# Optimization experiments

Measured on AMD Instinct MI355X. Metric: run time of the kernel, lower is better.

Reference implementation:

```python
import jax, jax.numpy as jnp
import numpy as np

THRESHOLD = 0.5
NEG_POS_RATIO = 3
ALPHA = 1.0


def cxcy_to_xy(c):
    # (cx,cy,w,h) -> (xmin,ymin,xmax,ymax)
    return jnp.concatenate([c[..., :2] - c[..., 2:] / 2.0,
                            c[..., :2] + c[..., 2:] / 2.0], axis=-1)


def gcxgcy_to_cxcy(g, priors):
    # standard SSD decode with variances (10, 5)
    return jnp.concatenate([g[..., :2] * priors[..., 2:] / 10.0 + priors[..., :2],
                            jnp.exp(g[..., 2:] / 5.0) * priors[..., 2:]], axis=-1)


def jaccard(set1, set2):
    # set1: [n1,4], set2: [n2,4], xyxy -> IoU matrix [n1,n2]
    lo = jnp.maximum(set1[:, None, :2], set2[None, :, :2])
    hi = jnp.minimum(set1[:, None, 2:], set2[None, :, 2:])
    wh = jnp.clip(hi - lo, 0.0)
    inter = wh[..., 0] * wh[..., 1]
    a1 = (set1[:, 2] - set1[:, 0]) * (set1[:, 3] - set1[:, 1])
    a2 = (set2[:, 2] - set2[:, 0]) * (set2[:, 3] - set2[:, 1])
    return inter / (a1[:, None] + a2[None, :] - inter)


def match_one(b, l, priors_xy):
    # b: [n_obj,4] GT boxes, l: [n_obj] labels, priors_xy: [P,4]
    n_obj = b.shape[0]
    ov = jaccard(b, priors_xy)                      # [n_obj, P]
    obj_for_prior = jnp.argmax(ov, axis=0)          # [P]
    ov_for_prior = jnp.max(ov, axis=0)              # [P]
    prior_for_obj = jnp.argmax(ov, axis=1)          # [n_obj]
    # force each object to own its best prior
    obj_for_prior = obj_for_prior.at[prior_for_obj].set(jnp.arange(n_obj))
    ov_for_prior = ov_for_prior.at[prior_for_obj].set(1.0)
    lab = l[obj_for_prior]
    lab = jnp.where(ov_for_prior < THRESHOLD, 0, lab)
    return lab, b[obj_for_prior]


def ciou(b1, b2):
    # elementwise CIoU over [..., 4] xyxy boxes -> [...]
    w1 = b1[..., 2] - b1[..., 0]; h1 = b1[..., 3] - b1[..., 1]
    w2 = b2[..., 2] - b2[..., 0]; h2 = b2[..., 3] - b2[..., 1]
    area1 = w1 * h1; area2 = w2 * h2
    cx1 = (b1[..., 2] + b1[..., 0]) / 2; cy1 = (b1[..., 3] + b1[..., 1]) / 2
    cx2 = (b2[..., 2] + b2[..., 0]) / 2; cy2 = (b2[..., 3] + b2[..., 1]) / 2
    in_wh = jnp.clip(jnp.minimum(b1[..., 2:], b2[..., 2:]) - jnp.maximum(b1[..., :2], b2[..., :2]), 0.0)
    out_wh = jnp.clip(jnp.maximum(b1[..., 2:], b2[..., 2:]) - jnp.minimum(b1[..., :2], b2[..., :2]), 0.0)
    inner_diag = (cx2 - cx1) ** 2 + (cy2 - cy1) ** 2
    outer_diag = out_wh[..., 0] ** 2 + out_wh[..., 1] ** 2
    inner = in_wh[..., 0] * in_wh[..., 1]
    iou = inner / (area1 + area2 - inner)
    v = (4.0 / (np.pi ** 2)) * (jnp.arctan(w2 / h2) - jnp.arctan(w1 / h1)) ** 2
    alpha = jax.lax.stop_gradient(v / (1.0 - iou + v))  # torch.no_grad()
    return 1.0 - iou + inner_diag / outer_diag + alpha * v


def setup_inputs() -> dict:
    key = jax.random.key(0)
    ks = jax.random.split(key, 7)
    N, P, C, NOBJ = 32, 8732, 81, 24
    predicted_locs = jax.random.normal(ks[0], (N, P, 4), jnp.float32)
    predicted_scores = jax.random.normal(ks[1], (N, P, C), jnp.float32)
    mins = jax.random.uniform(ks[2], (N, NOBJ, 2), minval=0.0, maxval=0.7)
    sizes = jax.random.uniform(ks[3], (N, NOBJ, 2), minval=0.05, maxval=0.3)
    boxes = jnp.concatenate([mins, mins + sizes], axis=-1)  # well-formed xyxy
    labels = jax.random.randint(ks[4], (N, NOBJ), 1, C)      # 1..C-1 (0 = background)
    pc = jax.random.uniform(ks[5], (P, 2), minval=0.05, maxval=0.95)
    pwh = jax.random.uniform(ks[6], (P, 2), minval=0.05, maxval=0.5)
    priors_cxcy = jnp.concatenate([pc, pwh], axis=-1)
    return {"predicted_locs": predicted_locs, "predicted_scores": predicted_scores,
            "boxes": boxes, "labels": labels, "priors_cxcy": priors_cxcy}


def reference(predicted_locs, predicted_scores, boxes, labels, priors_cxcy):
    priors_xy = cxcy_to_xy(priors_cxcy)
    # per-image GT->prior matching (vectorized over batch)
    true_classes, decoded_true = jax.vmap(match_one, in_axes=(0, 0, None))(boxes, labels, priors_xy)
    decoded_pred = cxcy_to_xy(gcxgcy_to_cxcy(predicted_locs, priors_cxcy[None]))  # [N,P,4]
    pos = true_classes != 0                              # [N,P]
    posf = pos.astype(predicted_locs.dtype)
    n_pos_total = jnp.sum(posf)
    # localization: CIoU mean over positive priors
    loc_loss = jnp.sum(ciou(decoded_pred, decoded_true) * posf) / n_pos_total
    # confidence: CE per prior
    logp = jax.nn.log_softmax(predicted_scores, axis=-1)
    conf_all = -jnp.take_along_axis(logp, true_classes[..., None], axis=-1)[..., 0]  # [N,P]
    conf_pos_sum = jnp.sum(conf_all * posf)
    # hard negative mining: top (neg_pos_ratio * n_pos) negatives per image
    conf_neg = jnp.where(pos, 0.0, conf_all)
    conf_neg_sorted = -jnp.sort(-conf_neg, axis=1)       # descending
    n_hard = NEG_POS_RATIO * jnp.sum(pos, axis=1)        # [N]
    ranks = jnp.arange(conf_neg_sorted.shape[1])[None, :]
    hard_mask = (ranks < n_hard[:, None]).astype(conf_all.dtype)
    conf_hard_neg_sum = jnp.sum(conf_neg_sorted * hard_mask)
    conf_loss = (conf_hard_neg_sum + conf_pos_sum) / n_pos_total
    return conf_loss + ALPHA * loc_loss
```

## Files before the change

### kernel.cpp

```cpp
#include <hip/hip_runtime.h>
#include <math.h>

#define BLK  256
#define BLKM 1024

constexpr int N_IMG = 32;
constexpr int P_PRI = 8732;
constexpr int C_CLS = 81;
constexpr int N_OBJ = 24;
constexpr int RPB   = 64;
constexpr int PB2   = (P_PRI + RPB - 1) / RPB;
constexpr int NBLK2 = PB2 * N_IMG;

__global__ void k_obj_match(const float* __restrict__ boxes,
                            const float* __restrict__ priors,
                            int* __restrict__ prior_for_obj,
                            int* __restrict__ npos) {
    const int o = blockIdx.x;
    const int n = blockIdx.y;
    const int tid = threadIdx.x;

    if (o == 0 && tid == 0) npos[n] = 0;

    const float x1 = boxes[(n * N_OBJ + o) * 4 + 0];
    const float y1 = boxes[(n * N_OBJ + o) * 4 + 1];
    const float x2 = boxes[(n * N_OBJ + o) * 4 + 2];
    const float y2 = boxes[(n * N_OBJ + o) * 4 + 3];
    const float ab = (x2 - x1) * (y2 - y1);

    const float4* pr4 = (const float4*)priors;

    float bv = -1.0f;
    int   bi = P_PRI;
    for (int p = tid; p < P_PRI; p += BLK) {
        const float4 c = pr4[p];
        const float px1 = c.x - c.z / 2.0f, py1 = c.y - c.w / 2.0f;
        const float px2 = c.x + c.z / 2.0f, py2 = c.y + c.w / 2.0f;
        const float pa  = (px2 - px1) * (py2 - py1);
        const float lox = fmaxf(x1, px1), loy = fmaxf(y1, py1);
        const float hix = fminf(x2, px2), hiy = fminf(y2, py2);
        const float iw = fmaxf(hix - lox, 0.0f), ih = fmaxf(hiy - loy, 0.0f);
        const float inter = iw * ih;
        const float iou = inter / (ab + pa - inter);
        if (iou > bv) { bv = iou; bi = p; }
    }

    __shared__ float sv[BLK];
    __shared__ int   si[BLK];
    sv[tid] = bv; si[tid] = bi;
    __syncthreads();
    for (int s = BLK / 2; s > 0; s >>= 1) {
        if (tid < s) {
            const float v2 = sv[tid + s]; const int i2 = si[tid + s];
            if (v2 > sv[tid] || (v2 == sv[tid] && i2 < si[tid])) { sv[tid] = v2; si[tid] = i2; }
        }
        __syncthreads();
    }
    if (tid == 0) prior_for_obj[n * N_OBJ + o] = si[0];
}

__global__ void __launch_bounds__(BLK)
k_main(const float* __restrict__ locs,
       const float* __restrict__ scores,
       const float* __restrict__ boxes,
       const int*   __restrict__ labels,
       const float* __restrict__ priors,
       const int*   __restrict__ prior_for_obj,
       float* __restrict__ conf_neg,
       int*   __restrict__ npos,
       float* __restrict__ partial_conf,
       float* __restrict__ partial_loc) {
    __shared__ int   pfo[N_OBJ];
    __shared__ int   slab[N_OBJ];
    __shared__ float wred[4][4];

    const int n   = blockIdx.y;
    const int r0  = blockIdx.x * RPB;
    const int tid = threadIdx.x;
    const int rows = min(RPB, P_PRI - r0);

    if (tid < N_OBJ) pfo[tid] = prior_for_obj[n * N_OBJ + tid];
    if (tid >= 64 && tid < 64 + N_OBJ) slab[tid - 64] = labels[n * N_OBJ + (tid - 64)];

    const int row = tid >> 2;
    const int q   = tid & 3;
    const int p   = r0 + row;
    const int psafe = (p < P_PRI) ? p : (P_PRI - 1);

    const float* xrow = scores + (size_t)(n * P_PRI + psafe) * C_CLS;
    float v[20];
#pragma unroll
    for (int i = 0; i < 20; ++i) v[i] = xrow[q + 4 * i];
    float v80 = 0.0f;
    if (q == 0) v80 = xrow[80];

    const float4 c = ((const float4*)priors)[psafe];
    const float px1 = c.x - c.z / 2.0f, py1 = c.y - c.w / 2.0f;
    const float px2 = c.x + c.z / 2.0f, py2 = c.y + c.w / 2.0f;
    const float pa  = (px2 - px1) * (py2 - py1);

    const float4* bxg = (const float4*)(boxes + (size_t)n * N_OBJ * 4);
    float bv = -1.0f;
    int   bo = q * 6;
#pragma unroll
    for (int j = 0; j < 6; ++j) {
        const int o = q * 6 + j;
        const float4 b = bxg[o];
        const float lox = fmaxf(b.x, px1), loy = fmaxf(b.y, py1);
        const float hix = fminf(b.z, px2), hiy = fminf(b.w, py2);
        const float iw = fmaxf(hix - lox, 0.0f), ih = fmaxf(hiy - loy, 0.0f);
        const float inter = iw * ih;
        const float ab = (b.z - b.x) * (b.w - b.y);
        const float iou = inter / (ab + pa - inter);
        if (iou > bv) { bv = iou; bo = o; }
    }
#pragma unroll
    for (int m = 1; m < 4; m <<= 1) {
        const float v2 = __shfl_xor(bv, m);
        const int   o2 = __shfl_xor(bo, m);
        if (v2 > bv || (v2 == bv && o2 < bo)) { bv = v2; bo = o2; }
    }
    __syncthreads();

    int fo = -1;
#pragma unroll
    for (int j = 0; j < 6; ++j) {
        const int o = q * 6 + j;
        if (pfo[o] == p) fo = o;
    }
#pragma unroll
    for (int m = 1; m < 4; m <<= 1) fo = max(fo, __shfl_xor(fo, m));

    const int   obj = (fo >= 0) ? fo : bo;
    const float ov  = (fo >= 0) ? 1.0f : bv;

    int cls = slab[obj];
    if (ov < 0.5f) cls = 0;

    float a0 = 0.0f, a1 = 0.0f, sel = 0.0f;
#pragma unroll
    for (int i = 0; i < 20; ++i) {
        const int cc = q + 4 * i;
        const float e = __expf(v[i]);
        if (i & 1) a1 += e; else a0 += e;
        sel += (cc == cls) ? v[i] : 0.0f;
    }
    float s = a0 + a1;
    if (q == 0) {
        s += __expf(v80);
        sel += (cls == 80) ? v80 : 0.0f;
    }
    s   += __shfl_xor(s, 1);
    s   += __shfl_xor(s, 2);
    sel += __shfl_xor(sel, 1);
    sel += __shfl_xor(sel, 2);

    float confpos = 0.0f, locv = 0.0f;
    int   cnt1 = 0;
    if (q == 0 && row < rows) {
        const float conf = __logf(s) - sel;
        const bool pos = (cls != 0);
        conf_neg[n * P_PRI + p] = pos ? 0.0f : fmaxf(conf, 0.0f);
        if (pos) {
            cnt1 = 1;
            confpos = conf;
            const float4 g = ((const float4*)locs)[(size_t)n * P_PRI + p];
            const float cx = g.x * c.z / 10.0f + c.x;
            const float cy = g.y * c.w / 10.0f + c.y;
            const float w  = expf(g.z / 5.0f) * c.z;
            const float hh = expf(g.w / 5.0f) * c.w;
            const float b1x1 = cx - w / 2.0f, b1y1 = cy - hh / 2.0f;
            const float b1x2 = cx + w / 2.0f, b1y2 = cy + hh / 2.0f;

            const float4 tb = bxg[obj];
            const float w1 = b1x2 - b1x1, h1 = b1y2 - b1y1;
            const float w2 = tb.z - tb.x, h2 = tb.w - tb.y;
            const float area1 = w1 * h1,  area2 = w2 * h2;
            const float c1x = (b1x2 + b1x1) / 2.0f, c1y = (b1y2 + b1y1) / 2.0f;
            const float c2x = (tb.z + tb.x) / 2.0f, c2y = (tb.w + tb.y) / 2.0f;
            const float inw = fmaxf(fminf(b1x2, tb.z) - fmaxf(b1x1, tb.x), 0.0f);
            const float inh = fmaxf(fminf(b1y2, tb.w) - fmaxf(b1y1, tb.y), 0.0f);
            const float owd = fmaxf(fmaxf(b1x2, tb.z) - fminf(b1x1, tb.x), 0.0f);
            const float ohd = fmaxf(fmaxf(b1y2, tb.w) - fminf(b1y1, tb.y), 0.0f);
            const float inner_diag = (c2x - c1x) * (c2x - c1x) + (c2y - c1y) * (c2y - c1y);
            const float outer_diag = owd * owd + ohd * ohd;
            const float inner = inw * inh;
            const float iou = inner / (area1 + area2 - inner);
            const float K = 0.40528473456935108577551785283891f;
            const float dat = atanf(w2 / h2) - atanf(w1 / h1);
            const float vv = K * dat * dat;
            const float alpha = vv / (1.0f - iou + vv);
            locv = 1.0f - iou + inner_diag / outer_diag + alpha * vv;
        }
    }

#pragma unroll
    for (int off = 32; off > 0; off >>= 1) {
        confpos += __shfl_down(confpos, off);
        locv    += __shfl_down(locv, off);
        cnt1    += __shfl_down(cnt1, off);
    }
    const int wid = tid >> 6;
    if ((tid & 63) == 0) {
        wred[wid][0] = confpos; wred[wid][1] = locv; wred[wid][2] = (float)cnt1;
    }
    __syncthreads();
    if (tid == 0) {
        float a = 0.0f, b = 0.0f, d = 0.0f;
#pragma unroll
        for (int w2 = 0; w2 < 4; ++w2) { a += wred[w2][0]; b += wred[w2][1]; d += wred[w2][2]; }
        const int slot = n * gridDim.x + blockIdx.x;
        partial_conf[slot] = a;
        partial_loc [slot] = b;
        atomicAdd(&npos[n], (int)d);
    }
}

__global__ void __launch_bounds__(BLKM)
k_mine(const float* __restrict__ conf_neg,
       const int*   __restrict__ npos,
       float* __restrict__ hardneg) {
    __shared__ int   wcnt[2][BLKM / 64];
    __shared__ float wsum[BLKM / 64];

    const int n    = blockIdx.x;
    const int tid  = threadIdx.x;
    const int wid  = tid >> 6;
    const int lane = tid & 63;

    unsigned v[9];
#pragma unroll
    for (int k = 0; k < 9; ++k) {
        const int p = tid + k * BLKM;
        v[k] = (p < P_PRI) ? __float_as_uint(conf_neg[n * P_PRI + p]) : 0u;
    }

    int k0 = 3 * npos[n];
    if (k0 > P_PRI) k0 = P_PRI;
    if (k0 <= 0) { if (tid == 0) hardneg[n] = 0.0f; return; }

    unsigned prefix = 0u;
    int kk = k0;
    for (int bit = 30; bit >= 0; --bit) {
        const unsigned hi = (prefix >> bit) | 1u;
        int cnt = 0;
#pragma unroll
        for (int k = 0; k < 9; ++k)
            cnt += __popcll(__ballot((v[k] >> bit) == hi));
        if (lane == 0) wcnt[bit & 1][wid] = cnt;
        __syncthreads();
        int tot = 0;
#pragma unroll
        for (int w = 0; w < BLKM / 64; ++w) tot += wcnt[bit & 1][w];
        if (tot >= kk) prefix |= (1u << bit);
        else           kk -= tot;
    }

    float psum = 0.0f; int pcnt = 0;
#pragma unroll
    for (int k = 0; k < 9; ++k) {
        if (v[k] > prefix) { psum += __uint_as_float(v[k]); ++pcnt; }
    }
#pragma unroll
    for (int off = 32; off > 0; off >>= 1) {
        psum += __shfl_down(psum, off);
        pcnt += __shfl_down(pcnt, off);
    }
    __syncthreads();
    if (lane == 0) { wsum[wid] = psum; wcnt[0][wid] = pcnt; }
    __syncthreads();
    if (tid == 0) {
        float S = 0.0f; int C = 0;
#pragma unroll
        for (int w = 0; w < BLKM / 64; ++w) { S += wsum[w]; C += wcnt[0][w]; }
        hardneg[n] = S + (float)(k0 - C) * __uint_as_float(prefix);
    }
}

__global__ void k_final(const float* __restrict__ partial_conf,
                        const float* __restrict__ partial_loc,
                        const int*   __restrict__ npos,
                        const float* __restrict__ hardneg,
                        float* __restrict__ out) {
    __shared__ float s1[BLK], s2[BLK], s3[BLK];
    __shared__ int   si[BLK];
    const int tid = threadIdx.x;

    float c = 0.0f, l = 0.0f, h = 0.0f;
    int np = 0;
    for (int i = tid; i < NBLK2; i += BLK) { c += partial_conf[i]; l += partial_loc[i]; }
    if (tid < N_IMG) { h = hardneg[tid]; np = npos[tid]; }

    s1[tid] = c; s2[tid] = l; s3[tid] = h; si[tid] = np;
    __syncthreads();
    for (int s = BLK / 2; s > 0; s >>= 1) {
        if (tid < s) { s1[tid] += s1[tid + s]; s2[tid] += s2[tid + s];
                       s3[tid] += s3[tid + s]; si[tid] += si[tid + s]; }
        __syncthreads();
    }
    if (tid == 0) {
        const float npt = (float)si[0];
        const float conf_loss = (s3[0] + s1[0]) / npt;
        const float loc_loss  = s2[0] / npt;
        out[0] = conf_loss + loc_loss;
    }
}

extern "C" void kernel_launch(void* const* d_in, const int* in_sizes, int n_in,
                              void* d_out, int out_size, void* d_ws, size_t ws_size,
                              hipStream_t stream) {
    const float* locs   = (const float*)d_in[0];
    const float* scores = (const float*)d_in[1];
    const float* boxes  = (const float*)d_in[2];
    const int*   labels = (const int*)  d_in[3];
    const float* priors = (const float*)d_in[4];
    float* out = (float*)d_out;

    char* w = (char*)d_ws;
    float* conf_neg      = (float*)w; w += (size_t)N_IMG * P_PRI * 4;
    int*   prior_for_obj = (int*)w;   w += (size_t)N_IMG * N_OBJ * 4;
    int*   npos          = (int*)w;   w += (size_t)N_IMG * 4;
    float* partial_conf  = (float*)w; w += (size_t)NBLK2 * 4;
    float* partial_loc   = (float*)w; w += (size_t)NBLK2 * 4;
    float* hardneg       = (float*)w; w += (size_t)N_IMG * 4;

    dim3 gridO(N_OBJ, N_IMG);
    k_obj_match<<<gridO, BLK, 0, stream>>>(boxes, priors, prior_for_obj, npos);

    dim3 gridM(PB2, N_IMG);
    k_main<<<gridM, BLK, 0, stream>>>(locs, scores, boxes, labels, priors,
                                      prior_for_obj, conf_neg, npos,
                                      partial_conf, partial_loc);

    k_mine<<<N_IMG, BLKM, 0, stream>>>(conf_neg, npos, hardneg);

    k_final<<<1, BLK, 0, stream>>>(partial_conf, partial_loc, npos, hardneg, out);
}
```

Before: 86.03 us.

## Fuse final reduction into mining kernel and use 8 lanes per prior

Removes the separate final-reduction launch by having the last mining block, found with an atomic counter and thread fences, do the global sum. The main kernel now gives each prior 8 lanes instead of 4, halving per-thread score registers and adding launch bounds for higher occupancy. It also swaps expf for the fast __expf in the box decode. The cost is more shuffle steps and twice as many blocks in the main kernel, plus slightly lower exp precision.

```diff
diff --git a/kernel.cpp b/kernel.cpp
--- a/kernel.cpp
+++ b/kernel.cpp
@@ -8,19 +8,22 @@
 constexpr int P_PRI = 8732;
 constexpr int C_CLS = 81;
 constexpr int N_OBJ = 24;
-constexpr int RPB   = 64;
+constexpr int LPR   = 8;
+constexpr int RPB   = BLK / LPR;
 constexpr int PB2   = (P_PRI + RPB - 1) / RPB;
 constexpr int NBLK2 = PB2 * N_IMG;
 
 __global__ void k_obj_match(const float* __restrict__ boxes,
                             const float* __restrict__ priors,
                             int* __restrict__ prior_for_obj,
-                            int* __restrict__ npos) {
+                            int* __restrict__ npos,
+                            int* __restrict__ done) {
     const int o = blockIdx.x;
     const int n = blockIdx.y;
     const int tid = threadIdx.x;
 
     if (o == 0 && tid == 0) npos[n] = 0;
+    if (o == 0 && n == 0 && tid == 1) *done = 0;
 
     const float x1 = boxes[(n * N_OBJ + o) * 4 + 0];
     const float y1 = boxes[(n * N_OBJ + o) * 4 + 1];
@@ -59,7 +62,7 @@
     if (tid == 0) prior_for_obj[n * N_OBJ + o] = si[0];
 }
 
-__global__ void __launch_bounds__(BLK)
+__global__ void __launch_bounds__(BLK, 8)
 k_main(const float* __restrict__ locs,
        const float* __restrict__ scores,
        const float* __restrict__ boxes,
@@ -82,17 +85,16 @@
     if (tid < N_OBJ) pfo[tid] = prior_for_obj[n * N_OBJ + tid];
     if (tid >= 64 && tid < 64 + N_OBJ) slab[tid - 64] = labels[n * N_OBJ + (tid - 64)];
 
-    const int row = tid >> 2;
-    const int q   = tid & 3;
+    const int row = tid >> 3;
+    const int q   = tid & 7;
     const int p   = r0 + row;
     const int psafe = (p < P_PRI) ? p : (P_PRI - 1);
 
     const float* xrow = scores + (size_t)(n * P_PRI + psafe) * C_CLS;
-    float v[20];
-#pragma unroll
-    for (int i = 0; i < 20; ++i) v[i] = xrow[q + 4 * i];
-    float v80 = 0.0f;
-    if (q == 0) v80 = xrow[80];
+    float v[10];
+#pragma unroll
+    for (int i = 0; i < 10; ++i) v[i] = xrow[q + 8 * i];
+    const float v80 = (q == 0) ? xrow[80] : 0.0f;
 
     const float4 c = ((const float4*)priors)[psafe];
     const float px1 = c.x - c.z / 2.0f, py1 = c.y - c.w / 2.0f;
@@ -101,10 +103,10 @@
 
     const float4* bxg = (const float4*)(boxes + (size_t)n * N_OBJ * 4);
     float bv = -1.0f;
-    int   bo = q * 6;
-#pragma unroll
-    for (int j = 0; j < 6; ++j) {
-        const int o = q * 6 + j;
+    int   bo = q * 3;
+#pragma unroll
+    for (int j = 0; j < 3; ++j) {
+        const int o = q * 3 + j;
         const float4 b = bxg[o];
         const float lox = fmaxf(b.x, px1), loy = fmaxf(b.y, py1);
         const float hix = fminf(b.z, px2), hiy = fminf(b.w, py2);
@@ -115,7 +117,7 @@
         if (iou > bv) { bv = iou; bo = o; }
     }
 #pragma unroll
-    for (int m = 1; m < 4; m <<= 1) {
+    for (int m = 1; m < 8; m <<= 1) {
         const float v2 = __shfl_xor(bv, m);
         const int   o2 = __shfl_xor(bo, m);
         if (v2 > bv || (v2 == bv && o2 < bo)) { bv = v2; bo = o2; }
@@ -124,12 +126,12 @@
 
     int fo = -1;
 #pragma unroll
-    for (int j = 0; j < 6; ++j) {
-        const int o = q * 6 + j;
+    for (int j = 0; j < 3; ++j) {
+        const int o = q * 3 + j;
         if (pfo[o] == p) fo = o;
     }
 #pragma unroll
-    for (int m = 1; m < 4; m <<= 1) fo = max(fo, __shfl_xor(fo, m));
+    for (int m = 1; m < 8; m <<= 1) fo = max(fo, __shfl_xor(fo, m));
 
     const int   obj = (fo >= 0) ? fo : bo;
     const float ov  = (fo >= 0) ? 1.0f : bv;
@@ -139,8 +141,8 @@
 
     float a0 = 0.0f, a1 = 0.0f, sel = 0.0f;
 #pragma unroll
-    for (int i = 0; i < 20; ++i) {
-        const int cc = q + 4 * i;
+    for (int i = 0; i < 10; ++i) {
+        const int cc = q + 8 * i;
         const float e = __expf(v[i]);
         if (i & 1) a1 += e; else a0 += e;
         sel += (cc == cls) ? v[i] : 0.0f;
@@ -150,10 +152,11 @@
         s += __expf(v80);
         sel += (cls == 80) ? v80 : 0.0f;
     }
-    s   += __shfl_xor(s, 1);
-    s   += __shfl_xor(s, 2);
-    sel += __shfl_xor(sel, 1);
-    sel += __shfl_xor(sel, 2);
+#pragma unroll
+    for (int m = 1; m < 8; m <<= 1) {
+        s   += __shfl_xor(s, m);
+        sel += __shfl_xor(sel, m);
+    }
 
     float confpos = 0.0f, locv = 0.0f;
     int   cnt1 = 0;
@@ -167,8 +170,8 @@
             const float4 g = ((const float4*)locs)[(size_t)n * P_PRI + p];
             const float cx = g.x * c.z / 10.0f + c.x;
             const float cy = g.y * c.w / 10.0f + c.y;
-            const float w  = expf(g.z / 5.0f) * c.z;
-            const float hh = expf(g.w / 5.0f) * c.w;
+            const float w  = __expf(g.z / 5.0f) * c.z;
+            const float hh = __expf(g.w / 5.0f) * c.w;
             const float b1x1 = cx - w / 2.0f, b1y1 = cy - hh / 2.0f;
             const float b1x2 = cx + w / 2.0f, b1y2 = cy + hh / 2.0f;
 
@@ -219,9 +222,16 @@
 __global__ void __launch_bounds__(BLKM)
 k_mine(const float* __restrict__ conf_neg,
        const int*   __restrict__ npos,
-       float* __restrict__ hardneg) {
+       float* __restrict__ hardneg,
+       const float* __restrict__ partial_conf,
+       const float* __restrict__ partial_loc,
+       int* __restrict__ done,
+       float* __restrict__ out) {
     __shared__ int   wcnt[2][BLKM / 64];
     __shared__ float wsum[BLKM / 64];
+    __shared__ float fs1[BLKM / 64], fs2[BLKM / 64], fs3[BLKM / 64];
+    __shared__ int   fi[BLKM / 64];
+    __shared__ bool  amLast;
 
     const int n    = blockIdx.x;
     const int tid  = threadIdx.x;
@@ -237,72 +247,73 @@
 
     int k0 = 3 * npos[n];
     if (k0 > P_PRI) k0 = P_PRI;
-    if (k0 <= 0) { if (tid == 0) hardneg[n] = 0.0f; return; }
-
-    unsigned prefix = 0u;
-    int kk = k0;
-    for (int bit = 30; bit >= 0; --bit) {
-        const unsigned hi = (prefix >> bit) | 1u;
-        int cnt = 0;
-#pragma unroll
-        for (int k = 0; k < 9; ++k)
-            cnt += __popcll(__ballot((v[k] >> bit) == hi));
-        if (lane == 0) wcnt[bit & 1][wid] = cnt;
+
+    float result = 0.0f;
+    if (k0 > 0) {
+        unsigned prefix = 0u;
+        int kk = k0;
+        for (int bit = 30; bit >= 0; --bit) {
+            const unsigned hi = (prefix >> bit) | 1u;
+            int cnt = 0;
+#pragma unroll
+            for (int k = 0; k < 9; ++k)
+                cnt += __popcll(__ballot((v[k] >> bit) == hi));
+            if (lane == 0) wcnt[bit & 1][wid] = cnt;
+            __syncthreads();
+            int tot = 0;
+#pragma unroll
+            for (int w = 0; w < BLKM / 64; ++w) tot += wcnt[bit & 1][w];
+            if (tot >= kk) prefix |= (1u << bit);
+            else           kk -= tot;
+        }
+
+        float psum = 0.0f; int pcnt = 0;
+#pragma unroll
+        for (int k = 0; k < 9; ++k) {
+            if (v[k] > prefix) { psum += __uint_as_float(v[k]); ++pcnt; }
+        }
+#pragma unroll
+        for (int off = 32; off > 0; off >>= 1) {
+            psum += __shfl_down(psum, off);
+            pcnt += __shfl_down(pcnt, off);
+        }
         __syncthreads();
-        int tot = 0;
-#pragma unroll
-        for (int w = 0; w < BLKM / 64; ++w) tot += wcnt[bit & 1][w];
-        if (tot >= kk) prefix |= (1u << bit);
-        else           kk -= tot;
-    }
-
-    float psum = 0.0f; int pcnt = 0;
-#pragma unroll
-    for (int k = 0; k < 9; ++k) {
-        if (v[k] > prefix) { psum += __uint_as_float(v[k]); ++pcnt; }
-    }
-#pragma unroll
-    for (int off = 32; off > 0; off >>= 1) {
-        psum += __shfl_down(psum, off);
-        pcnt += __shfl_down(pcnt, off);
-    }
-    __syncthreads();
-    if (lane == 0) { wsum[wid] = psum; wcnt[0][wid] = pcnt; }
-    __syncthreads();
-    if (tid == 0) {
-        float S = 0.0f; int C = 0;
-#pragma unroll
-        for (int w = 0; w < BLKM / 64; ++w) { S += wsum[w]; C += wcnt[0][w]; }
-        hardneg[n] = S + (float)(k0 - C) * __uint_as_float(prefix);
-    }
-}
-
-__global__ void k_final(const float* __restrict__ partial_conf,
-                        const float* __restrict__ partial_loc,
-                        const int*   __restrict__ npos,
-                        const float* __restrict__ hardneg,
-                        float* __restrict__ out) {
-    __shared__ float s1[BLK], s2[BLK], s3[BLK];
-    __shared__ int   si[BLK];
-    const int tid = threadIdx.x;
+        if (lane == 0) { wsum[wid] = psum; wcnt[0][wid] = pcnt; }
+        __syncthreads();
+        if (tid == 0) {
+            float S = 0.0f; int C = 0;
+#pragma unroll
+            for (int w = 0; w < BLKM / 64; ++w) { S += wsum[w]; C += wcnt[0][w]; }
+            result = S + (float)(k0 - C) * __uint_as_float(prefix);
+        }
+    }
+    if (tid == 0) hardneg[n] = result;
+
+    __threadfence();
+    if (tid == 0) amLast = (atomicAdd(done, 1) == N_IMG - 1);
+    __syncthreads();
+    if (!amLast) return;
+    __threadfence();
 
     float c = 0.0f, l = 0.0f, h = 0.0f;
     int np = 0;
-    for (int i = tid; i < NBLK2; i += BLK) { c += partial_conf[i]; l += partial_loc[i]; }
+    for (int i = tid; i < NBLK2; i += BLKM) { c += partial_conf[i]; l += partial_loc[i]; }
     if (tid < N_IMG) { h = hardneg[tid]; np = npos[tid]; }
-
-    s1[tid] = c; s2[tid] = l; s3[tid] = h; si[tid] = np;
-    __syncthreads();
-    for (int s = BLK / 2; s > 0; s >>= 1) {
-        if (tid < s) { s1[tid] += s1[tid + s]; s2[tid] += s2[tid + s];
-                       s3[tid] += s3[tid + s]; si[tid] += si[tid + s]; }
-        __syncthreads();
-    }
+#pragma unroll
+    for (int off = 32; off > 0; off >>= 1) {
+        c  += __shfl_down(c, off);
+        l  += __shfl_down(l, off);
+        h  += __shfl_down(h, off);
+        np += __shfl_down(np, off);
+    }
+    if (lane == 0) { fs1[wid] = c; fs2[wid] = l; fs3[wid] = h; fi[wid] = np; }
+    __syncthreads();
     if (tid == 0) {
-        const float npt = (float)si[0];
-        const float conf_loss = (s3[0] + s1[0]) / npt;
-        const float loc_loss  = s2[0] / npt;
-        out[0] = conf_loss + loc_loss;
+        float C = 0.0f, L = 0.0f, H = 0.0f; int NP = 0;
+#pragma unroll
+        for (int w = 0; w < BLKM / 64; ++w) { C += fs1[w]; L += fs2[w]; H += fs3[w]; NP += fi[w]; }
+        const float npt = (float)NP;
+        out[0] = (H + C) / npt + L / npt;
     }
 }
 
@@ -323,16 +334,16 @@
     float* partial_conf  = (float*)w; w += (size_t)NBLK2 * 4;
     float* partial_loc   = (float*)w; w += (size_t)NBLK2 * 4;
     float* hardneg       = (float*)w; w += (size_t)N_IMG * 4;
+    int*   done          = (int*)w;   w += 64;
 
     dim3 gridO(N_OBJ, N_IMG);
-    k_obj_match<<<gridO, BLK, 0, stream>>>(boxes, priors, prior_for_obj, npos);
+    k_obj_match<<<gridO, BLK, 0, stream>>>(boxes, priors, prior_for_obj, npos, done);
 
     dim3 gridM(PB2, N_IMG);
     k_main<<<gridM, BLK, 0, stream>>>(locs, scores, boxes, labels, priors,
                                       prior_for_obj, conf_neg, npos,
                                       partial_conf, partial_loc);
 
-    k_mine<<<N_IMG, BLKM, 0, stream>>>(conf_neg, npos, hardneg);
-
-    k_final<<<1, BLK, 0, stream>>>(partial_conf, partial_loc, npos, hardneg, out);
+    k_mine<<<N_IMG, BLKM, 0, stream>>>(conf_neg, npos, hardneg,
+                                       partial_conf, partial_loc, done, out);
 }
```

Measured after the change: 131.8 us. 53.2% more time.
